# Performance work log

Hardware: AMD Instinct MI355X
Metric: run time of the kernel (lower is better)

The kernel has to match this reference:

```python
import jax, jax.numpy as jnp
import numpy as np

DIM = 256
HEADS = 8
DIM_HEAD = 64
EPS = 1e-12  # F.normalize eps


def rms_norm(x, w, dim):
    # F.normalize over channel dim (axis=1) * weight * sqrt(dim)
    n = jnp.sqrt(jnp.sum(x * x, axis=1, keepdims=True))
    xn = x / jnp.maximum(n, EPS)
    return xn * w[None, :, None, None] * (dim ** 0.5)


def setup_inputs() -> dict:
    key = jax.random.key(0)
    ks = jax.random.split(key, 4)
    hd = HEADS * DIM_HEAD
    return {
        "x": jax.random.normal(ks[0], (16, DIM, 64, 64), dtype=jnp.float32),
        "norm_w": jnp.ones((DIM,), jnp.float32),
        "qkv_w": jax.random.normal(ks[1], (3 * hd, DIM), jnp.float32) * (DIM ** -0.5),
        "out_w": jax.random.normal(ks[2], (DIM, hd), jnp.float32) * (hd ** -0.5),
        "out_b": jnp.zeros((DIM,), jnp.float32),
        "out_norm_w": jnp.ones((DIM,), jnp.float32),
    }


def reference(x, norm_w, qkv_w, out_w, out_b, out_norm_w):
    b, c, H, W = x.shape
    n = H * W
    scale = DIM_HEAD ** -0.5

    xn = rms_norm(x, norm_w, DIM)
    # 1x1 conv == channel matmul: [3hd, c] x [b, c, H, W]
    qkv = jnp.einsum('oc,bchw->bohw', qkv_w, xn)
    q, k, v = jnp.split(qkv, 3, axis=1)

    def to_heads(t):
        # b (h d) x y -> b h d n
        return t.reshape(b, HEADS, DIM_HEAD, n)

    q = jax.nn.softmax(to_heads(q), axis=2) * scale  # softmax over feature dim d
    k = jax.nn.softmax(to_heads(k), axis=3)          # softmax over spatial n
    v = to_heads(v)

    ctx = jnp.einsum('bhdn,bhen->bhde', k, v)   # [b,h,d,e]
    out = jnp.einsum('bhde,bhdn->bhen', ctx, q) # [b,h,e,n]
    out = out.reshape(b, HEADS * DIM_HEAD, H, W)

    out = jnp.einsum('oc,bchw->bohw', out_w, out) + out_b[None, :, None, None]
    return rms_norm(out, out_norm_w, DIM)
```

## Files before the change

kernel.cpp:

```cpp
#include <hip/hip_runtime.h>

#define C_ 256
#define N_ 4096
#define NH_ 8

typedef unsigned short u16;
typedef unsigned int u32;
typedef __attribute__((ext_vector_type(8))) short s8v;
typedef __attribute__((ext_vector_type(4))) float f4v;

#define MFMA16 __builtin_amdgcn_mfma_f32_16x16x32_bf16

__device__ __forceinline__ float bf2f(u16 b){ union{u32 u; float f;} v; v.u=((u32)b)<<16; return v.f; }
__device__ __forceinline__ u16 f2bf(float f){ union{float f; u32 u;} v; v.f=f; return (u16)((v.u + 0x7FFFu + ((v.u>>16)&1u))>>16); }

__device__ __forceinline__ void gl_lds16(const u16* g, u16* l){
  __builtin_amdgcn_global_load_lds((const __attribute__((address_space(1))) u32*)g,
                                   (__attribute__((address_space(3))) u32*)l, 16, 0, 0);
}

__global__ __launch_bounds__(256) void k_prep(const float* __restrict__ x, const float* __restrict__ nw,
                                              u16* __restrict__ xnT){
  __shared__ float red[256];
  __shared__ float nws[256];
  const int tid = threadIdx.x;
  nws[tid] = nw[tid];
  const int blk = blockIdx.x, b = blk>>6, n0 = (blk&63)*64;
  const int cq = tid>>6, px = tid&63;
  const float* xp = x + (size_t)b*(C_*N_) + (size_t)(cq*64)*N_ + n0 + px;
  float v[64]; float s = 0.f;
  #pragma unroll
  for (int i=0;i<64;i++){ float t = xp[(size_t)i*N_]; v[i]=t; s = fmaf(t,t,s); }
  red[tid] = s;
  __syncthreads();
  const float st = red[px] + red[64+px] + red[128+px] + red[192+px];
  const float r = 16.0f / fmaxf(sqrtf(st), 1e-12f);
  u16* o = xnT + ((size_t)b*4096 + n0 + px)*256 + cq*64;
  #pragma unroll
  for (int i=0;i<64;i+=2){
    *(u32*)(o+i) = (u32)f2bf(v[i]*r*nws[cq*64+i]) | ((u32)f2bf(v[i+1]*r*nws[cq*64+i+1])<<16);
  }
}

__global__ __launch_bounds__(256) void k_wconv(const float* __restrict__ qkvw, const float* __restrict__ ow,
                                               u16* __restrict__ wqkv, u16* __restrict__ owb){
  int i = blockIdx.x*256 + threadIdx.x;
  if (i < 393216) wqkv[i] = f2bf(qkvw[i]);
  else            owb[i-393216] = f2bf(ow[i-393216]);
}

__global__ __launch_bounds__(256,3) void k_kv(const u16* __restrict__ xnT, const u16* __restrict__ wqkv,
    u16* __restrict__ ctxp, float* __restrict__ Mp, float* __restrict__ Sp){
  __shared__ u16 xs[64*256];
  __shared__ u16 pbuf[64*72];
  __shared__ u16 vbuf[64*72];
  const int idx = blockIdx.x;
  const int ch = idx&7, h = (idx>>3)&7, b = idx>>6;
  const int tid=threadIdx.x, w=tid>>6, l=tid&63, l15=l&15, lg=l>>4;
  const int swl = (l15&7)<<4;
  const u16* xb  = xnT + (size_t)b*(4096*256);
  const int srow = (l>>5);
  const int scolB = (l&31)*16;
  s8v ak[8], av[8];
  {
    const u16* wkp = wqkv + (size_t)(512 + h*64 + w*16 + l15)*256 + lg*8;
    #pragma unroll
    for (int cs=0; cs<8; cs++){ ak[cs] = *(const s8v*)(wkp + cs*32); av[cs] = *(const s8v*)(wkp + 131072 + cs*32); }
  }
  int colOff[8];
  #pragma unroll
  for (int cs=0; cs<8; cs++) colOff[cs] = (((cs<<6)+(lg<<4)) ^ swl)>>1;

  f4v acc[4];
  #pragma unroll
  for (int et=0;et<4;et++) acc[et] = (f4v){0.f,0.f,0.f,0.f};
  float ps[4] = {0.f,0.f,0.f,0.f};

  {
    const int n0 = ch*512;
    #pragma unroll
    for (int i=0;i<8;i++){
      int rloc = w*16 + i*2 + srow;
      int scol = scolB ^ ((rloc&7)<<4);
      gl_lds16(xb + (size_t)(n0+rloc)*256 + (scol>>1), &xs[(w*16+i*2)*256]);
    }
  }

  for (int t=0; t<8; ++t){
    __syncthreads();
    f4v kacc[4], vacc[4];
    #pragma unroll
    for (int ns=0;ns<4;ns++){ kacc[ns]=(f4v){0.f,0.f,0.f,0.f}; vacc[ns]=(f4v){0.f,0.f,0.f,0.f}; }
    #pragma unroll
    for (int cs=0; cs<8; cs++){
      #pragma unroll
      for (int ns=0; ns<4; ns++){
        s8v bfr = *(const s8v*)&xs[(ns*16+l15)*256 + colOff[cs]];
        kacc[ns] = MFMA16(ak[cs], bfr, kacc[ns], 0,0,0);
        vacc[ns] = MFMA16(av[cs], bfr, vacc[ns], 0,0,0);
      }
    }
    #pragma unroll
    for (int j=0;j<4;j++){
      const int row = w*16 + lg*4 + j;
      #pragma unroll
      for (int ns=0;ns<4;ns++){
        float e = __expf(kacc[ns][j] - 30.0f);
        ps[j] += e;
        pbuf[row*72 + ns*16+l15] = f2bf(e);
        vbuf[row*72 + ns*16+l15] = f2bf(vacc[ns][j]);
      }
    }
    __syncthreads();
    if (t<7){
      const int n0 = ch*512 + (t+1)*64;
      #pragma unroll
      for (int i=0;i<8;i++){
        int rloc = w*16 + i*2 + srow;
        int scol = scolB ^ ((rloc&7)<<4);
        gl_lds16(xb + (size_t)(n0+rloc)*256 + (scol>>1), &xs[(w*16+i*2)*256]);
      }
    }
    #pragma unroll
    for (int ks=0; ks<2; ks++){
      s8v af = *(const s8v*)(pbuf + (w*16+l15)*72 + ks*32 + lg*8);
      #pragma unroll
      for (int et=0; et<4; et++){
        s8v bv = *(const s8v*)(vbuf + (et*16+l15)*72 + ks*32 + lg*8);
        acc[et] = MFMA16(af, bv, acc[et], 0,0,0);
      }
    }
  }
  u16* cp = ctxp + (((size_t)ch*16 + b)*8 + h)*4096;
  #pragma unroll
  for (int et=0; et<4; et++)
    #pragma unroll
    for (int j=0;j<4;j++)
      cp[(w*16+lg*4+j)*64 + et*16+l15] = f2bf(acc[et][j]);
  #pragma unroll
  for (int j=0;j<4;j++){
    float s = ps[j];
    s += __shfl_xor(s,1); s += __shfl_xor(s,2);
    s += __shfl_xor(s,4); s += __shfl_xor(s,8);
    ps[j] = s;
  }
  if (l15==0){
    #pragma unroll
    for (int j=0;j<4;j++){
      int rg = (b*8+h)*64 + w*16 + lg*4 + j;
      Mp[ch*8192+rg]=30.0f; Sp[ch*8192+rg]=ps[j];
    }
  }
}

__global__ __launch_bounds__(256) void k_comb(const u16* __restrict__ ctxp, const float* __restrict__ Mp,
    const float* __restrict__ Sp, u16* __restrict__ ctxT){
  __shared__ float fs[8][64];
  __shared__ float iSs[64];
  const int bh = blockIdx.x, tid = threadIdx.x;
  if (tid < 64){
    float m[8];
    float Mg = -1e30f;
    #pragma unroll
    for (int ch=0;ch<8;ch++){ m[ch] = Mp[ch*8192 + bh*64 + tid]; Mg = fmaxf(Mg, m[ch]); }
    float Sg = 0.f;
    #pragma unroll
    for (int ch=0;ch<8;ch++){
      float fv = __expf(m[ch]-Mg);
      fs[ch][tid] = fv;
      Sg += Sp[ch*8192 + bh*64 + tid]*fv;
    }
    iSs[tid] = 1.0f / Sg;
  }
  __syncthreads();
  const int e = tid>>2, d0 = (tid&3)*16;
  u16* op = ctxT + (size_t)bh*4096 + e*64 + d0;
  #pragma unroll
  for (int i=0;i<16;i++){
    int d = d0+i;
    float v = 0.f;
    #pragma unroll
    for (int ch=0;ch<8;ch++)
      v += bf2f(ctxp[((size_t)(ch*128)+bh)*4096 + d*64 + e]) * fs[ch][d];
    op[i] = f2bf(v * iSs[d]);
  }
}

__global__ __launch_bounds__(256,2) void k_qout(const u16* __restrict__ xnT, const u16* __restrict__ wqkv,
    const u16* __restrict__ owb, const u16* __restrict__ ctxT,
    const float* __restrict__ ob, const float* __restrict__ onw, float* __restrict__ out){
  __shared__ u16 WQ[64*256];
  __shared__ u16 OWs[256*64];
  __shared__ u16 qa[4][16*80];
  __shared__ float obs[256], onws[256];
  const int tid = threadIdx.x;
  obs[tid]=ob[tid]; onws[tid]=onw[tid];
  __syncthreads();
  const int w=tid>>6, l=tid&63, l15=l&15, lg=l>>4;
  const int swl = (l15&7)<<4;
  const int blk=blockIdx.x, b=blk>>6, n0=(blk&63)*64 + w*16;
  const u16* xb = xnT + ((size_t)b*4096 + n0)*256;
  u16* qaw = qa[w];
  s8v ax[8];
  #pragma unroll
  for (int cs=0;cs<8;cs++) ax[cs] = *(const s8v*)(xb + (size_t)l15*256 + cs*32 + lg*8);
  f4v oacc[16];
  #pragma unroll
  for (int mt=0;mt<16;mt++) oacc[mt] = (f4v){0.f,0.f,0.f,0.f};

  for (int h=0; h<8; ++h){
    __syncthreads();
    {
      const u16* wqg = wqkv + (size_t)h*64*256;
      #pragma unroll
      for (int i=0;i<8;i++){
        int row = w*16 + i*2 + (l>>5);
        int colB = (l&31)*16;
        int scol = colB ^ ((row&7)<<4);
        gl_lds16(wqg + row*256 + (scol>>1), &WQ[(w*16 + i*2)*256]);
      }
    }
    {
      #pragma unroll
      for (int i=0;i<8;i++){
        int row = w*64 + i*8 + (l>>3);
        int colB = (l&7)*16;
        int scol = colB ^ ((row&7)<<4);
        gl_lds16(owb + (size_t)row*512 + h*64 + (scol>>1), &OWs[(w*64 + i*8)*64]);
      }
    }
    s8v bc[8];
    {
      const u16* cxb = ctxT + ((size_t)(b*8+h))*4096;
      #pragma unroll
      for (int ks=0; ks<2; ks++)
        #pragma unroll
        for (int et=0; et<4; et++)
          bc[ks*4+et] = *(const s8v*)(cxb + (et*16+l15)*64 + ks*32 + lg*8);
    }
    __syncthreads();
    f4v qacc[4];
    #pragma unroll
    for (int dt=0;dt<4;dt++) qacc[dt] = (f4v){0.f,0.f,0.f,0.f};
    #pragma unroll
    for (int dt=0; dt<4; dt++){
      #pragma unroll
      for (int cs=0; cs<8; cs++){
        s8v bw = *(const s8v*)&WQ[(dt*16+l15)*256 + ((((cs<<6)+(lg<<4)) ^ swl)>>1)];
        qacc[dt] = MFMA16(ax[cs], bw, qacc[dt], 0,0,0);
      }
    }
    #pragma unroll
    for (int j=0;j<4;j++){
      float m = fmaxf(fmaxf(qacc[0][j],qacc[1][j]),fmaxf(qacc[2][j],qacc[3][j]));
      #pragma unroll
      for (int d=1; d<16; d<<=1) m = fmaxf(m, __shfl_xor(m, d));
      float s = 0.f;
      #pragma unroll
      for (int dt=0;dt<4;dt++){ float e=__expf(qacc[dt][j]-m); qacc[dt][j]=e; s+=e; }
      #pragma unroll
      for (int d=1; d<16; d<<=1) s += __shfl_xor(s, d);
      float inv = 0.125f/s;
      #pragma unroll
      for (int dt=0;dt<4;dt++) qaw[(lg*4+j)*80 + dt*16+l15] = f2bf(qacc[dt][j]*inv);
    }
    f4v aacc[4];
    #pragma unroll
    for (int et=0;et<4;et++) aacc[et] = (f4v){0.f,0.f,0.f,0.f};
    #pragma unroll
    for (int ks=0; ks<2; ks++){
      s8v aq = *(const s8v*)&qaw[l15*80 + ks*32 + lg*8];
      #pragma unroll
      for (int et=0; et<4; et++)
        aacc[et] = MFMA16(aq, bc[ks*4+et], aacc[et], 0,0,0);
    }
    #pragma unroll
    for (int et=0;et<4;et++)
      #pragma unroll
      for (int j=0;j<4;j++)
        qaw[(lg*4+j)*80 + et*16+l15] = f2bf(aacc[et][j]);
    #pragma unroll
    for (int ks=0; ks<2; ks++){
      s8v ba = *(const s8v*)&qaw[l15*80 + ks*32 + lg*8];
      #pragma unroll
      for (int mt=0; mt<16; mt++){
        s8v aw = *(const s8v*)&OWs[(mt*16+l15)*64 + ((((ks<<6)+(lg<<4)) ^ swl)>>1)];
        oacc[mt] = MFMA16(aw, ba, oacc[mt], 0,0,0);
      }
    }
  }
  float ss = 0.f;
  #pragma unroll
  for (int mt=0;mt<16;mt++)
    #pragma unroll
    for (int j=0;j<4;j++){
      float v = oacc[mt][j] + obs[mt*16+lg*4+j];
      oacc[mt][j] = v;
      ss = fmaf(v,v,ss);
    }
  ss += __shfl_xor(ss, 16);
  ss += __shfl_xor(ss, 32);
  const float r = 16.0f / fmaxf(sqrtf(ss), 1e-12f);
  float* op = out + (size_t)b*(256*4096) + n0 + l15;
  #pragma unroll
  for (int mt=0;mt<16;mt++)
    #pragma unroll
    for (int j=0;j<4;j++){
      int cout = mt*16+lg*4+j;
      op[(size_t)cout*4096] = oacc[mt][j] * r * onws[cout];
    }
}

extern "C" void kernel_launch(void* const* d_in, const int* in_sizes, int n_in,
                              void* d_out, int out_size, void* d_ws, size_t ws_size,
                              hipStream_t stream){
  const float* x    = (const float*)d_in[0];
  const float* nw   = (const float*)d_in[1];
  const float* qkvw = (const float*)d_in[2];
  const float* ow   = (const float*)d_in[3];
  const float* ob   = (const float*)d_in[4];
  const float* onw  = (const float*)d_in[5];
  float* out = (float*)d_out;
  char* ws = (char*)d_ws;
  u16*   xnT  = (u16*)(ws);
  u16*   wqkv = (u16*)(ws + 33554432);
  u16*   owb  = (u16*)(ws + 34340864);
  u16*   ctxT = (u16*)(ws + 34603008);
  u16*   ctxp = (u16*)(ws + 35651584);
  float* Mp   = (float*)(ws + 44040192);
  float* Sp   = (float*)(ws + 44302336);
  (void)in_sizes; (void)n_in; (void)out_size; (void)ws_size;

  k_wconv<<<2048, 256, 0, stream>>>(qkvw, ow, wqkv, owb);
  k_prep <<<1024, 256, 0, stream>>>(x, nw, xnT);
  k_kv   <<<1024, 256, 0, stream>>>(xnT, wqkv, ctxp, Mp, Sp);
  k_comb <<<128, 256, 0, stream>>>(ctxp, Mp, Sp, ctxT);
  k_qout <<<1024, 256, 0, stream>>>(xnT, wqkv, owb, ctxT, ob, onw, out);
}
```

Measured before the change: 178.6 us.

## Double-buffer per-head weight tiles and double block size in k_qout

Per-head WQ and output-weight tiles are now double-buffered in LDS, so the next head's tiles are loaded asynchronously while the current head computes. This removes the barrier that exposed load latency each iteration. Blocks grow to 512 threads covering 128 spatial positions, which halves the weight traffic per output. The cost is much higher LDS use per block, which limits residency to one block per CU, and the qa row padding is changed.

Result: faster. 173.7 us (-2.7%).

```diff
diff --git a/kernel.cpp b/kernel.cpp
--- a/kernel.cpp
+++ b/kernel.cpp
@@ -186,21 +186,25 @@
   }
 }
 
-__global__ __launch_bounds__(256,2) void k_qout(const u16* __restrict__ xnT, const u16* __restrict__ wqkv,
+__global__ __launch_bounds__(512,2) void k_qout(const u16* __restrict__ xnT, const u16* __restrict__ wqkv,
     const u16* __restrict__ owb, const u16* __restrict__ ctxT,
     const float* __restrict__ ob, const float* __restrict__ onw, float* __restrict__ out){
-  __shared__ u16 WQ[64*256];
-  __shared__ u16 OWs[256*64];
-  __shared__ u16 qa[4][16*80];
+  __shared__ u16 WQb[2][64*256];
+  __shared__ u16 OWb[2][256*64];
+  __shared__ u16 qa[8][16*72];
   __shared__ float obs[256], onws[256];
   const int tid = threadIdx.x;
-  obs[tid]=ob[tid]; onws[tid]=onw[tid];
-  __syncthreads();
+  if (tid < 256){ obs[tid]=ob[tid]; onws[tid]=onw[tid]; }
   const int w=tid>>6, l=tid&63, l15=l&15, lg=l>>4;
   const int swl = (l15&7)<<4;
-  const int blk=blockIdx.x, b=blk>>6, n0=(blk&63)*64 + w*16;
+  const int blk=blockIdx.x, b=blk>>5, n0=(blk&31)*128 + w*16;
   const u16* xb = xnT + ((size_t)b*4096 + n0)*256;
+  const u16* cxb0 = ctxT + ((size_t)b*8)*4096;
   u16* qaw = qa[w];
+  const int wqRowB = w*8 + (l>>5);
+  const int wqColB = (l&31)*16;
+  const int owRowB = w*32 + (l>>3);
+  const int owColB = (l&7)*16;
   s8v ax[8];
   #pragma unroll
   for (int cs=0;cs<8;cs++) ax[cs] = *(const s8v*)(xb + (size_t)l15*256 + cs*32 + lg*8);
@@ -208,37 +212,51 @@
   #pragma unroll
   for (int mt=0;mt<16;mt++) oacc[mt] = (f4v){0.f,0.f,0.f,0.f};
 
+  {
+    const u16* wqg = wqkv;
+    #pragma unroll
+    for (int i=0;i<4;i++){
+      int row = wqRowB + i*2;
+      int scol = wqColB ^ ((row&7)<<4);
+      gl_lds16(wqg + (size_t)row*256 + (scol>>1), &WQb[0][(w*8+i*2)*256]);
+    }
+    #pragma unroll
+    for (int i=0;i<4;i++){
+      int row = owRowB + i*8;
+      int scol = owColB ^ ((row&7)<<4);
+      gl_lds16(owb + (size_t)row*512 + 0 + (scol>>1), &OWb[0][(w*32+i*8)*64]);
+    }
+  }
+
   for (int h=0; h<8; ++h){
-    __syncthreads();
-    {
-      const u16* wqg = wqkv + (size_t)h*64*256;
-      #pragma unroll
-      for (int i=0;i<8;i++){
-        int row = w*16 + i*2 + (l>>5);
-        int colB = (l&31)*16;
-        int scol = colB ^ ((row&7)<<4);
-        gl_lds16(wqg + row*256 + (scol>>1), &WQ[(w*16 + i*2)*256]);
-      }
-    }
-    {
-      #pragma unroll
-      for (int i=0;i<8;i++){
-        int row = w*64 + i*8 + (l>>3);
-        int colB = (l&7)*16;
-        int scol = colB ^ ((row&7)<<4);
-        gl_lds16(owb + (size_t)row*512 + h*64 + (scol>>1), &OWs[(w*64 + i*8)*64]);
-      }
-    }
+    const int p = h&1;
+    asm volatile("s_waitcnt vmcnt(0)" ::: "memory");
+    __builtin_amdgcn_s_barrier();
+    __builtin_amdgcn_sched_barrier(0);
     s8v bc[8];
     {
-      const u16* cxb = ctxT + ((size_t)(b*8+h))*4096;
+      const u16* cxb = cxb0 + (size_t)h*4096;
       #pragma unroll
       for (int ks=0; ks<2; ks++)
         #pragma unroll
         for (int et=0; et<4; et++)
           bc[ks*4+et] = *(const s8v*)(cxb + (et*16+l15)*64 + ks*32 + lg*8);
     }
-    __syncthreads();
+    if (h<7){
+      const u16* wqg = wqkv + (size_t)(h+1)*64*256;
+      #pragma unroll
+      for (int i=0;i<4;i++){
+        int row = wqRowB + i*2;
+        int scol = wqColB ^ ((row&7)<<4);
+        gl_lds16(wqg + (size_t)row*256 + (scol>>1), &WQb[p^1][(w*8+i*2)*256]);
+      }
+      #pragma unroll
+      for (int i=0;i<4;i++){
+        int row = owRowB + i*8;
+        int scol = owColB ^ ((row&7)<<4);
+        gl_lds16(owb + (size_t)row*512 + (h+1)*64 + (scol>>1), &OWb[p^1][(w*32+i*8)*64]);
+      }
+    }
     f4v qacc[4];
     #pragma unroll
     for (int dt=0;dt<4;dt++) qacc[dt] = (f4v){0.f,0.f,0.f,0.f};
@@ -246,7 +264,7 @@
     for (int dt=0; dt<4; dt++){
       #pragma unroll
       for (int cs=0; cs<8; cs++){
-        s8v bw = *(const s8v*)&WQ[(dt*16+l15)*256 + ((((cs<<6)+(lg<<4)) ^ swl)>>1)];
+        s8v bw = *(const s8v*)&WQb[p][(dt*16+l15)*256 + ((((cs<<6)+(lg<<4)) ^ swl)>>1)];
         qacc[dt] = MFMA16(ax[cs], bw, qacc[dt], 0,0,0);
       }
     }
@@ -262,14 +280,14 @@
       for (int d=1; d<16; d<<=1) s += __shfl_xor(s, d);
       float inv = 0.125f/s;
       #pragma unroll
-      for (int dt=0;dt<4;dt++) qaw[(lg*4+j)*80 + dt*16+l15] = f2bf(qacc[dt][j]*inv);
+      for (int dt=0;dt<4;dt++) qaw[(lg*4+j)*72 + dt*16+l15] = f2bf(qacc[dt][j]*inv);
     }
     f4v aacc[4];
     #pragma unroll
     for (int et=0;et<4;et++) aacc[et] = (f4v){0.f,0.f,0.f,0.f};
     #pragma unroll
     for (int ks=0; ks<2; ks++){
-      s8v aq = *(const s8v*)&qaw[l15*80 + ks*32 + lg*8];
+      s8v aq = *(const s8v*)&qaw[l15*72 + ks*32 + lg*8];
       #pragma unroll
       for (int et=0; et<4; et++)
         aacc[et] = MFMA16(aq, bc[ks*4+et], aacc[et], 0,0,0);
@@ -278,13 +296,13 @@
     for (int et=0;et<4;et++)
       #pragma unroll
       for (int j=0;j<4;j++)
-        qaw[(lg*4+j)*80 + et*16+l15] = f2bf(aacc[et][j]);
+        qaw[(lg*4+j)*72 + et*16+l15] = f2bf(aacc[et][j]);
     #pragma unroll
     for (int ks=0; ks<2; ks++){
-      s8v ba = *(const s8v*)&qaw[l15*80 + ks*32 + lg*8];
+      s8v ba = *(const s8v*)&qaw[l15*72 + ks*32 + lg*8];
       #pragma unroll
       for (int mt=0; mt<16; mt++){
-        s8v aw = *(const s8v*)&OWs[(mt*16+l15)*64 + ((((ks<<6)+(lg<<4)) ^ swl)>>1)];
+        s8v aw = *(const s8v*)&OWb[p][(mt*16+l15)*64 + ((((ks<<6)+(lg<<4)) ^ swl)>>1)];
         oacc[mt] = MFMA16(aw, ba, oacc[mt], 0,0,0);
       }
     }
@@ -335,5 +353,5 @@
   k_prep <<<1024, 256, 0, stream>>>(x, nw, xnT);
   k_kv   <<<1024, 256, 0, stream>>>(xnT, wqkv, ctxp, Mp, Sp);
   k_comb <<<128, 256, 0, stream>>>(ctxp, Mp, Sp, ctxT);
-  k_qout <<<1024, 256, 0, stream>>>(xnT, wqkv, owb, ctxT, ob, onw, out);
-}
+  k_qout <<<512, 512, 0, stream>>>(xnT, wqkv, owb, ctxT, ob, onw, out);
+}
```
